# Kernel optimization log

Hardware: AMD Instinct MI355X
Metric: run time of the kernel (lower is better)

## Reference

```python
import jax, jax.numpy as jnp
import numpy as np

NUM_VOXELS = 2_000_000
NUM_CLUSTS = 2000
NUM_EDGES = 16_000
IN_FEATS = 4      # columns 1:5 of data: x, y, z, value
HIDDEN = 128
LATENT = 64       # encoder output feature size


def setup_inputs() -> dict:
    key = jax.random.key(0)
    k1, k2, k3, k4, k5, k6, k7 = jax.random.split(key, 7)
    data = jax.random.normal(k1, (NUM_VOXELS, 5), dtype=jnp.float32)
    clust_ids = jax.random.randint(k2, (NUM_VOXELS,), 0, NUM_CLUSTS)
    edge_index = jax.random.randint(k3, (2, NUM_EDGES), 0, NUM_CLUSTS)
    # encoder (pool + MLP) parameters
    W1 = jax.random.normal(k4, (IN_FEATS, HIDDEN), dtype=jnp.float32) / np.sqrt(IN_FEATS)
    b1 = jnp.zeros((HIDDEN,), dtype=jnp.float32)
    W2 = jax.random.normal(k5, (HIDDEN, LATENT), dtype=jnp.float32) / np.sqrt(HIDDEN)
    b2 = jnp.zeros((LATENT,), dtype=jnp.float32)
    return {"data": data, "clust_ids": clust_ids, "edge_index": edge_index,
            "W1": W1, "b1": b1, "W2": W2, "b2": b2}


def reference(data, clust_ids, edge_index, W1, b1, W2, b2):
    # Vectorized replacement of the per-edge python loop:
    # the loop builds, per edge i, the union of voxels of clusters (e0, e1)
    # with batch column overwritten by i; the encoder then globally pools
    # per edge-id. Equivalent: per-cluster sums via one segment_sum pass,
    # then per-edge mean over the union of the two clusters.
    feat = data[:, 1:5]                                   # [N, 4]
    clust_sum = jax.ops.segment_sum(feat, clust_ids, num_segments=NUM_CLUSTS)  # [C, 4]
    clust_cnt = jax.ops.segment_sum(jnp.ones((data.shape[0],), dtype=feat.dtype),
                                    clust_ids, num_segments=NUM_CLUSTS)        # [C]
    e0, e1 = edge_index[0], edge_index[1]
    pooled = (clust_sum[e0] + clust_sum[e1]) / jnp.maximum(clust_cnt[e0] + clust_cnt[e1], 1.0)[:, None]  # [E, 4]
    h = jax.nn.relu(pooled @ W1 + b1)                     # [E, HIDDEN]
    feats = h @ W2 + b2                                   # [E, LATENT]
    return feats
```

## Files before the change

### kernel.cpp

```cpp
#include <hip/hip_runtime.h>

#define NUM_VOXELS 2000000
#define NUM_CLUSTS 2000
#define NUM_EDGES  16000

#define ST   2048
#define ACCN (5 * ST)

#define FSCALE  65536.0f
#define FINV    (1.0f / 65536.0f)
#define BIASF   8.0f
#define BIAS_FS (8.0f * 65536.0f)

#define A_BLOCKS  256
#define A_THREADS 1024
#define RED_CH    64
#define NCH       (A_BLOCKS / RED_CH)

typedef float  f4v __attribute__((ext_vector_type(4)));
typedef int    i4v __attribute__((ext_vector_type(4)));
typedef unsigned long long u64;

__device__ __forceinline__ u64 pack2(float a, float b) {
    unsigned lo = (unsigned)__float2int_rn(fmaf(a, FSCALE, BIAS_FS));
    unsigned hi = (unsigned)__float2int_rn(fmaf(b, FSCALE, BIAS_FS));
    return (u64)lo | ((u64)hi << 32);
}

__global__ __launch_bounds__(A_THREADS) void seg_accum(
        const float* __restrict__ data,
        const int* __restrict__ cids,
        int* __restrict__ part) {
    __shared__ __align__(16) int ls[ACCN];
    u64* s01 = (u64*)ls;
    u64* s23 = (u64*)(ls + 4096);
    int* scnt = ls + 8192;
    for (int o = threadIdx.x; o < ACCN; o += A_THREADS) ls[o] = 0;
    __syncthreads();

    const int ngroups = NUM_VOXELS / 4;
    for (int g = blockIdx.x * A_THREADS + threadIdx.x; g < ngroups;
         g += gridDim.x * A_THREADS) {
        const f4v* dp = (const f4v*)(data + 20ull * (unsigned)g);
        f4v q0 = dp[0];
        f4v q1 = dp[1];
        f4v q2 = dp[2];
        f4v q3 = dp[3];
        f4v q4 = dp[4];
        i4v c4 = *(const i4v*)(cids + 4ull * (unsigned)g);

        atomicAdd(&s01[c4.x], pack2(q0.y, q0.z));
        atomicAdd(&s23[c4.x], pack2(q0.w, q1.x));
        atomicAdd(&scnt[c4.x], 1);
        atomicAdd(&s01[c4.y], pack2(q1.z, q1.w));
        atomicAdd(&s23[c4.y], pack2(q2.x, q2.y));
        atomicAdd(&scnt[c4.y], 1);
        atomicAdd(&s01[c4.z], pack2(q2.w, q3.x));
        atomicAdd(&s23[c4.z], pack2(q3.y, q3.z));
        atomicAdd(&scnt[c4.z], 1);
        atomicAdd(&s01[c4.w], pack2(q4.x, q4.y));
        atomicAdd(&s23[c4.w], pack2(q4.z, q4.w));
        atomicAdd(&scnt[c4.w], 1);
    }
    __syncthreads();

    int* p = part + (size_t)blockIdx.x * ACCN;
    for (int o = threadIdx.x; o < ACCN; o += A_THREADS) p[o] = ls[o];
}

__global__ __launch_bounds__(A_THREADS) void seg_accum_atomic(
        const float* __restrict__ data,
        const int* __restrict__ cids,
        int* __restrict__ acc) {
    __shared__ __align__(16) int ls[ACCN];
    u64* s01 = (u64*)ls;
    u64* s23 = (u64*)(ls + 4096);
    int* scnt = ls + 8192;
    for (int o = threadIdx.x; o < ACCN; o += A_THREADS) ls[o] = 0;
    __syncthreads();
    const int ngroups = NUM_VOXELS / 4;
    for (int g = blockIdx.x * A_THREADS + threadIdx.x; g < ngroups;
         g += gridDim.x * A_THREADS) {
        const f4v* dp = (const f4v*)(data + 20ull * (unsigned)g);
        f4v q0 = dp[0], q1 = dp[1], q2 = dp[2], q3 = dp[3], q4 = dp[4];
        i4v c4 = *(const i4v*)(cids + 4ull * (unsigned)g);
        atomicAdd(&s01[c4.x], pack2(q0.y, q0.z));
        atomicAdd(&s23[c4.x], pack2(q0.w, q1.x));
        atomicAdd(&scnt[c4.x], 1);
        atomicAdd(&s01[c4.y], pack2(q1.z, q1.w));
        atomicAdd(&s23[c4.y], pack2(q2.x, q2.y));
        atomicAdd(&scnt[c4.y], 1);
        atomicAdd(&s01[c4.z], pack2(q2.w, q3.x));
        atomicAdd(&s23[c4.z], pack2(q3.y, q3.z));
        atomicAdd(&scnt[c4.z], 1);
        atomicAdd(&s01[c4.w], pack2(q4.x, q4.y));
        atomicAdd(&s23[c4.w], pack2(q4.z, q4.w));
        atomicAdd(&scnt[c4.w], 1);
    }
    __syncthreads();
    for (int o = threadIdx.x; o < ACCN; o += A_THREADS) {
        int v = ls[o];
        if (v != 0) atomicAdd(&acc[o], v);
    }
}

__global__ __launch_bounds__(256) void seg_combine(int* __restrict__ part) {
    const int i = blockIdx.x * 256 + threadIdx.x;
    const int b0 = blockIdx.y * RED_CH + (blockIdx.y == 0 ? 1 : 0);
    const int b1 = blockIdx.y * RED_CH + RED_CH;
    int s = 0;
    for (int b = b0; b < b1; ++b) s += part[(size_t)b * ACCN + i];
    atomicAdd(&part[i], s);
}

#define E_BLOCKS 500
#define E_THREADS 256
#define EPW 8

__global__ __launch_bounds__(E_THREADS) void edge_mlp(
        const int* __restrict__ img,
        const int* __restrict__ eidx,
        const float* __restrict__ W1, const float* __restrict__ b1,
        const float* __restrict__ W2, const float* __restrict__ b2,
        float* __restrict__ out) {
    __shared__ float hbuf[E_THREADS / 64][2][128];
    const int lane = threadIdx.x & 63;
    const int w = threadIdx.x >> 6;
    const int wg = blockIdx.x * (E_THREADS / 64) + w;
    const int ebase = wg * EPW;

    float w1a[4], w1b[4];
#pragma unroll
    for (int c = 0; c < 4; ++c) {
        w1a[c] = W1[c * 128 + lane];
        w1b[c] = W1[c * 128 + 64 + lane];
    }
    const float b1a = b1[lane];
    const float b1b = b1[64 + lane];
    const float b2j = b2[lane];
    float w2c[128];
#pragma unroll
    for (int k = 0; k < 128; ++k) w2c[k] = W2[k * 64 + lane];

    int ids0[EPW], ids1[EPW];
    {
        i4v a = *(const i4v*)&eidx[ebase];
        i4v b = *(const i4v*)&eidx[ebase + 4];
        ids0[0] = a.x; ids0[1] = a.y; ids0[2] = a.z; ids0[3] = a.w;
        ids0[4] = b.x; ids0[5] = b.y; ids0[6] = b.z; ids0[7] = b.w;
        i4v c = *(const i4v*)&eidx[NUM_EDGES + ebase];
        i4v d = *(const i4v*)&eidx[NUM_EDGES + ebase + 4];
        ids1[0] = c.x; ids1[1] = c.y; ids1[2] = c.z; ids1[3] = c.w;
        ids1[4] = d.x; ids1[5] = d.y; ids1[6] = d.z; ids1[7] = d.w;
    }

#pragma unroll
    for (int i = 0; i < EPW; ++i) {
        const int e0 = ids0[i], e1 = ids1[i];
        const i4v fa = {img[2 * e0], img[2 * e0 + 1],
                        img[4096 + 2 * e0], img[4096 + 2 * e0 + 1]};
        const i4v fb = {img[2 * e1], img[2 * e1 + 1],
                        img[4096 + 2 * e1], img[4096 + 2 * e1 + 1]};
        const float cnt = (float)img[8192 + e0] + (float)img[8192 + e1];
        const float rden = 1.0f / fmaxf(cnt, 1.0f);
        const float bt = -BIASF * cnt;
        const float p0 = fmaf((float)fa.x + (float)fb.x, FINV, bt) * rden;
        const float p1 = fmaf((float)fa.y + (float)fb.y, FINV, bt) * rden;
        const float p2 = fmaf((float)fa.z + (float)fb.z, FINV, bt) * rden;
        const float p3 = fmaf((float)fa.w + (float)fb.w, FINV, bt) * rden;

        float ha = b1a + p0 * w1a[0] + p1 * w1a[1] + p2 * w1a[2] + p3 * w1a[3];
        float hb = b1b + p0 * w1b[0] + p1 * w1b[1] + p2 * w1b[2] + p3 * w1b[3];
        ha = fmaxf(ha, 0.0f);
        hb = fmaxf(hb, 0.0f);

        float* hx = hbuf[w][i & 1];
        hx[lane] = ha;
        hx[64 + lane] = hb;

        float a0 = b2j, a1 = 0.f, a2 = 0.f, a3 = 0.f;
#pragma unroll
        for (int k = 0; k < 128; k += 16) {
            float4 h4;
            h4 = *(const float4*)&hx[k];
            a0 += h4.x * w2c[k] + h4.y * w2c[k + 1] + h4.z * w2c[k + 2] + h4.w * w2c[k + 3];
            h4 = *(const float4*)&hx[k + 4];
            a1 += h4.x * w2c[k + 4] + h4.y * w2c[k + 5] + h4.z * w2c[k + 6] + h4.w * w2c[k + 7];
            h4 = *(const float4*)&hx[k + 8];
            a2 += h4.x * w2c[k + 8] + h4.y * w2c[k + 9] + h4.z * w2c[k + 10] + h4.w * w2c[k + 11];
            h4 = *(const float4*)&hx[k + 12];
            a3 += h4.x * w2c[k + 12] + h4.y * w2c[k + 13] + h4.z * w2c[k + 14] + h4.w * w2c[k + 15];
        }
        out[(size_t)(ebase + i) * 64 + lane] = (a0 + a1) + (a2 + a3);
    }
}

extern "C" void kernel_launch(void* const* d_in, const int* in_sizes, int n_in,
                              void* d_out, int out_size, void* d_ws, size_t ws_size,
                              hipStream_t stream) {
    const float* data = (const float*)d_in[0];
    const int* cids   = (const int*)d_in[1];
    const int* eidx   = (const int*)d_in[2];
    const float* W1   = (const float*)d_in[3];
    const float* b1   = (const float*)d_in[4];
    const float* W2   = (const float*)d_in[5];
    const float* b2   = (const float*)d_in[6];
    float* out = (float*)d_out;
    int* ws = (int*)d_ws;

    if (ws_size >= (size_t)A_BLOCKS * ACCN * sizeof(int)) {
        int* part = ws;
        seg_accum<<<A_BLOCKS, A_THREADS, 0, stream>>>(data, cids, part);
        seg_combine<<<dim3(ACCN / 256, NCH), 256, 0, stream>>>(part);
        edge_mlp<<<E_BLOCKS, E_THREADS, 0, stream>>>(part, eidx, W1, b1, W2, b2, out);
    } else {
        int* img = ws;
        hipMemsetAsync(img, 0, ACCN * sizeof(int), stream);
        seg_accum_atomic<<<A_BLOCKS, A_THREADS, 0, stream>>>(data, cids, img);
        edge_mlp<<<E_BLOCKS, E_THREADS, 0, stream>>>(img, eidx, W1, b1, W2, b2, out);
    }
}
```

Measured before the change: 117.9 us.

## Fuse partial-sum combine and edge MLP into one cooperative kernel with grid sync

Replaces the separate seg_combine and edge_mlp launches with a single cooperative kernel. The first 160 blocks reduce the 256 per-block partial accumulators, a grid-wide sync follows, and then every block runs the edge MLP with 16 edges per wave. Edge indices and weights are loaded before the sync so their latency overlaps the reduction. The aim is to remove one kernel launch and the gap between kernels, at the cost of grid-sync overhead, fewer active waves for the MLP, and a more serialized reduction in which each wave walks 64 partials.

```diff
diff --git a/kernel.cpp b/kernel.cpp
--- a/kernel.cpp
+++ b/kernel.cpp
@@ -1,4 +1,7 @@
 #include <hip/hip_runtime.h>
+#include <hip/hip_cooperative_groups.h>
+
+namespace cg = cooperative_groups;
 
 #define NUM_VOXELS 2000000
 #define NUM_CLUSTS 2000
@@ -113,6 +116,111 @@
     atomicAdd(&part[i], s);
 }
 
+#define F_BLOCKS 256
+#define F_THREADS 256
+#define F_EPW 16
+#define F_ACT_WAVES (NUM_EDGES / F_EPW)
+#define F_CMB_BLOCKS (ACCN / 64)
+
+__global__ __launch_bounds__(F_THREADS) void combine_edge(
+        int* __restrict__ part,
+        const int* __restrict__ eidx,
+        const float* __restrict__ W1, const float* __restrict__ b1,
+        const float* __restrict__ W2, const float* __restrict__ b2,
+        float* __restrict__ out) {
+    __shared__ int red[4][64];
+    __shared__ float hbuf[F_THREADS / 64][2][128];
+    const int tid = threadIdx.x;
+    const int lane = tid & 63;
+    const int w = tid >> 6;
+
+    float w1a[4], w1b[4];
+#pragma unroll
+    for (int c = 0; c < 4; ++c) {
+        w1a[c] = W1[c * 128 + lane];
+        w1b[c] = W1[c * 128 + 64 + lane];
+    }
+    const float b1a = b1[lane];
+    const float b1b = b1[64 + lane];
+    const float b2j = b2[lane];
+    float w2c[128];
+#pragma unroll
+    for (int k = 0; k < 128; ++k) w2c[k] = W2[k * 64 + lane];
+
+    const int wg = blockIdx.x * (F_THREADS / 64) + w;
+    int ids0[F_EPW], ids1[F_EPW];
+    const int ebase = wg * F_EPW;
+    if (wg < F_ACT_WAVES) {
+#pragma unroll
+        for (int q = 0; q < F_EPW / 4; ++q) {
+            i4v a = *(const i4v*)&eidx[ebase + 4 * q];
+            ids0[4 * q] = a.x; ids0[4 * q + 1] = a.y;
+            ids0[4 * q + 2] = a.z; ids0[4 * q + 3] = a.w;
+            i4v b = *(const i4v*)&eidx[NUM_EDGES + ebase + 4 * q];
+            ids1[4 * q] = b.x; ids1[4 * q + 1] = b.y;
+            ids1[4 * q + 2] = b.z; ids1[4 * q + 3] = b.w;
+        }
+    }
+
+    if (blockIdx.x < F_CMB_BLOCKS) {
+        const int i = blockIdx.x * 64 + lane;
+        int s = 0;
+        for (int b = w * 64; b < w * 64 + 64; ++b)
+            if (b != 0) s += part[(size_t)b * ACCN + i];
+        red[w][lane] = s;
+    }
+    __syncthreads();
+    if (blockIdx.x < F_CMB_BLOCKS && tid < 64) {
+        const int i = blockIdx.x * 64 + tid;
+        part[i] += red[0][tid] + red[1][tid] + red[2][tid] + red[3][tid];
+    }
+    __threadfence();
+    cg::this_grid().sync();
+
+    if (wg < F_ACT_WAVES) {
+        const int* img = part;
+#pragma unroll
+        for (int i = 0; i < F_EPW; ++i) {
+            const int e0 = ids0[i], e1 = ids1[i];
+            const i4v fa = {img[2 * e0], img[2 * e0 + 1],
+                            img[4096 + 2 * e0], img[4096 + 2 * e0 + 1]};
+            const i4v fb = {img[2 * e1], img[2 * e1 + 1],
+                            img[4096 + 2 * e1], img[4096 + 2 * e1 + 1]};
+            const float cnt = (float)img[8192 + e0] + (float)img[8192 + e1];
+            const float rden = 1.0f / fmaxf(cnt, 1.0f);
+            const float bt = -BIASF * cnt;
+            const float p0 = fmaf((float)fa.x + (float)fb.x, FINV, bt) * rden;
+            const float p1 = fmaf((float)fa.y + (float)fb.y, FINV, bt) * rden;
+            const float p2 = fmaf((float)fa.z + (float)fb.z, FINV, bt) * rden;
+            const float p3 = fmaf((float)fa.w + (float)fb.w, FINV, bt) * rden;
+
+            float ha = b1a + p0 * w1a[0] + p1 * w1a[1] + p2 * w1a[2] + p3 * w1a[3];
+            float hb = b1b + p0 * w1b[0] + p1 * w1b[1] + p2 * w1b[2] + p3 * w1b[3];
+            ha = fmaxf(ha, 0.0f);
+            hb = fmaxf(hb, 0.0f);
+
+            float* hx = hbuf[w][i & 1];
+            hx[lane] = ha;
+            hx[64 + lane] = hb;
+
+            float a0 = b2j, a1 = 0.f, a2 = 0.f, a3 = 0.f;
+#pragma unroll
+            for (int k = 0; k < 128; k += 16) {
+                float4 h4;
+                h4 = *(const float4*)&hx[k];
+                a0 += h4.x * w2c[k] + h4.y * w2c[k + 1] + h4.z * w2c[k + 2] + h4.w * w2c[k + 3];
+                h4 = *(const float4*)&hx[k + 4];
+                a1 += h4.x * w2c[k + 4] + h4.y * w2c[k + 5] + h4.z * w2c[k + 6] + h4.w * w2c[k + 7];
+                h4 = *(const float4*)&hx[k + 8];
+                a2 += h4.x * w2c[k + 8] + h4.y * w2c[k + 9] + h4.z * w2c[k + 10] + h4.w * w2c[k + 11];
+                h4 = *(const float4*)&hx[k + 12];
+                a3 += h4.x * w2c[k + 12] + h4.y * w2c[k + 13] + h4.z * w2c[k + 14] + h4.w * w2c[k + 15];
+            }
+            out[(size_t)(ebase + i) * 64 + lane] = (a0 + a1) + (a2 + a3);
+        }
+    }
+}
+
 #define E_BLOCKS 500
 #define E_THREADS 256
 #define EPW 8
@@ -211,8 +319,17 @@
     if (ws_size >= (size_t)A_BLOCKS * ACCN * sizeof(int)) {
         int* part = ws;
         seg_accum<<<A_BLOCKS, A_THREADS, 0, stream>>>(data, cids, part);
-        seg_combine<<<dim3(ACCN / 256, NCH), 256, 0, stream>>>(part);
-        edge_mlp<<<E_BLOCKS, E_THREADS, 0, stream>>>(part, eidx, W1, b1, W2, b2, out);
+        void* args[] = {(void*)&part, (void*)&eidx, (void*)&W1, (void*)&b1,
+                        (void*)&W2, (void*)&b2, (void*)&out};
+        hipError_t ce = hipLaunchCooperativeKernel((void*)combine_edge,
+                                                   dim3(F_BLOCKS), dim3(F_THREADS),
+                                                   args, 0, stream);
+        if (ce != hipSuccess) {
+            (void)hipGetLastError();
+            seg_combine<<<dim3(ACCN / 256, NCH), 256, 0, stream>>>(part);
+            edge_mlp<<<E_BLOCKS, E_THREADS, 0, stream>>>(part, eidx, W1, b1, W2,
+                                                         b2, out);
+        }
     } else {
         int* img = ws;
         hipMemsetAsync(img, 0, ACCN * sizeof(int), stream);
```

After: 205.8 us. 1.75x slower.
